# Kernel tuning notes

Measured on AMD Instinct MI355X. Metric: run time of the kernel, lower is better.

Reference implementation:

```python
import jax, jax.numpy as jnp
import numpy as np

B, N, E = 8, 10000, 320000
IN_DIM, E_H, E_OUT, N_OUT = 16, 32, 22, 16


def setup_inputs() -> dict:
    key = jax.random.key(0)
    ks = jax.random.split(key, 8)
    x = jax.random.uniform(ks[0], (B, N, IN_DIM), dtype=jnp.float32)
    edge_index = jax.random.randint(ks[1], (2, E), 0, N, dtype=jnp.int64)
    # edge_attr: col 0 = city_dist (keep strictly positive), col 1 = city_direc
    ea = jax.random.uniform(ks[2], (E, 2), dtype=jnp.float32)
    edge_attr = jnp.stack([ea[:, 0] * 100.0 + 1.0, ea[:, 1] * 360.0], axis=-1)
    wind_min = jnp.array([0.0, 0.0], dtype=jnp.float32)
    wind_max = jnp.array([15.0, 360.0], dtype=jnp.float32)
    W1 = jax.random.normal(ks[3], (2 * IN_DIM + 2 + 1, E_H), dtype=jnp.float32) * 0.1
    b1 = jnp.zeros((E_H,), dtype=jnp.float32)
    W2 = jax.random.normal(ks[4], (E_H, E_OUT), dtype=jnp.float32) * 0.1
    b2 = jnp.zeros((E_OUT,), dtype=jnp.float32)
    Wn = jax.random.normal(ks[5], (E_OUT, N_OUT), dtype=jnp.float32) * 0.1
    bn = jnp.zeros((N_OUT,), dtype=jnp.float32)
    return {"x": x, "edge_index": edge_index, "edge_attr": edge_attr,
            "wind_min": wind_min, "wind_max": wind_max,
            "W1": W1, "b1": b1, "W2": W2, "b2": b2, "Wn": Wn, "bn": bn}


def reference(x, edge_index, edge_attr, wind_min, wind_max, W1, b1, W2, b2, Wn, bn):
    edge_src = edge_index[0]
    edge_tgt = edge_index[1]
    n_nodes = x.shape[1]

    node_src = x[:, edge_src]      # [B, E, F]
    node_tgt = x[:, edge_tgt]      # [B, E, F]

    # de-normalize the last two features (wind speed, wind direction)
    src_wind = node_src[..., -2:] * (wind_max - wind_min) + wind_min
    src_speed = src_wind[..., 0]   # [B, E]
    src_direc = src_wind[..., 1]   # [B, E]

    city_dist = edge_attr[:, 0]    # [E]
    city_direc = edge_attr[:, 1]   # [E]

    theta = jnp.abs(city_direc[None, :] - src_direc)
    edge_weight = jax.nn.relu(src_speed * jnp.cos(theta) / city_dist[None, :])  # [B, E]

    ea_min = edge_attr.min(axis=0)
    ea_max = edge_attr.max(axis=0)
    ea_norm = (edge_attr - ea_min) / (ea_max - ea_min)  # [E, 2]
    ea_norm_b = jnp.broadcast_to(ea_norm[None], (x.shape[0],) + ea_norm.shape)

    feat = jnp.concatenate([node_src, node_tgt, ea_norm_b, edge_weight[..., None]], axis=-1)  # [B, E, 35]

    h = jax.nn.sigmoid(feat @ W1 + b1)   # [B, E, 32]
    e = jax.nn.sigmoid(h @ W2 + b2)      # [B, E, 22]

    # scatter_add to target nodes, scatter_add of negated messages to source nodes
    agg = jnp.zeros((x.shape[0], n_nodes, e.shape[-1]), dtype=e.dtype)
    agg = agg.at[:, edge_tgt].add(e)
    agg = agg.at[:, edge_src].add(-e)

    return jax.nn.sigmoid(agg @ Wn + bn)  # [B, N, out_dim]
```

## Files before the change

### kernel.cpp

```cpp
#include <hip/hip_runtime.h>
#include <math.h>

#define BB 8
#define NN 10000
#define EE 320000
#define NCHUNK 128
#define CHSZ (EE / NCHUNK)

#define OFF_MM   0
#define OFF_WIND 16
#define OFF_PRE1 160016
#define OFF_PRE2 2720016
#define OFF_OFFP 5280016
#define OFF_TOT  5300018
#define OFF_MMP  5320018
#define OFF_CNTC 5320530
#define OFF_LST  7880530
#define OFF_G    8520544

__device__ __forceinline__ float sigmf(float x) {
    return __fdividef(1.0f, 1.0f + __expf(-x));
}


__global__ __launch_bounds__(256) void count_kernel(const int* __restrict__ ei,
                                                    const float* __restrict__ ea,
                                                    unsigned* __restrict__ cntc,
                                                    float* __restrict__ mmpart) {
    __shared__ unsigned hist[NN];
    __shared__ float mred[4][4];
    const int c = blockIdx.x, a = blockIdx.y, tid = threadIdx.x;
    for (int i = tid; i < NN; i += 256) hist[i] = 0u;
    __syncthreads();
    const int e0 = c * CHSZ;
    float n0 = 3.4e38f, n1 = 3.4e38f, x0 = 0.f, x1 = 0.f;
    for (int k = tid; k < CHSZ; k += 256) {
        int v = ei[(size_t)a * EE + e0 + k];
        atomicAdd(&hist[v], 1u);
        if (a == 0) {
            float2 av = ((const float2*)ea)[e0 + k];
            n0 = fminf(n0, av.x); x0 = fmaxf(x0, av.x);
            n1 = fminf(n1, av.y); x1 = fmaxf(x1, av.y);
        }
    }
    __syncthreads();
    unsigned* dst = cntc + ((size_t)a * NCHUNK + c) * NN;
    for (int i = tid; i < NN; i += 256) dst[i] = hist[i];
    if (a == 0) {
        #pragma unroll
        for (int off = 32; off >= 1; off >>= 1) {
            n0 = fminf(n0, __shfl_xor(n0, off)); n1 = fminf(n1, __shfl_xor(n1, off));
            x0 = fmaxf(x0, __shfl_xor(x0, off)); x1 = fmaxf(x1, __shfl_xor(x1, off));
        }
        int w = tid >> 6;
        if ((tid & 63) == 0) { mred[w][0] = n0; mred[w][1] = n1; mred[w][2] = x0; mred[w][3] = x1; }
        __syncthreads();
        if (tid == 0) {
            mmpart[c * 4 + 0] = fminf(fminf(mred[0][0], mred[1][0]), fminf(mred[2][0], mred[3][0]));
            mmpart[c * 4 + 1] = fminf(fminf(mred[0][1], mred[1][1]), fminf(mred[2][1], mred[3][1]));
            mmpart[c * 4 + 2] = fmaxf(fmaxf(mred[0][2], mred[1][2]), fmaxf(mred[2][2], mred[3][2]));
            mmpart[c * 4 + 3] = fmaxf(fmaxf(mred[0][3], mred[1][3]), fmaxf(mred[2][3], mred[3][3]));
        }
    }
}

__global__ __launch_bounds__(256) void tot_kernel(const unsigned* __restrict__ cntc,
                                                  unsigned* __restrict__ tot) {
    int v = blockIdx.x * 256 + threadIdx.x;
    int a = blockIdx.y;
    if (v >= NN) return;
    const unsigned* base = cntc + (size_t)a * NCHUNK * NN;
    unsigned s = 0;
    for (int c = 0; c < NCHUNK; c++) s += base[(size_t)c * NN + v];
    tot[a * NN + v] = s;
}

__global__ __launch_bounds__(1024) void scan_kernel(const unsigned* __restrict__ tot,
                                                    const float* __restrict__ mmpart,
                                                    unsigned* __restrict__ offp,
                                                    float* __restrict__ mmo) {
    __shared__ unsigned ts[1024];
    int t = threadIdx.x;
    if (t < 64) {
        float n0 = fminf(mmpart[4 * t + 0], mmpart[4 * (t + 64) + 0]);
        float n1 = fminf(mmpart[4 * t + 1], mmpart[4 * (t + 64) + 1]);
        float x0 = fmaxf(mmpart[4 * t + 2], mmpart[4 * (t + 64) + 2]);
        float x1 = fmaxf(mmpart[4 * t + 3], mmpart[4 * (t + 64) + 3]);
        #pragma unroll
        for (int off = 32; off >= 1; off >>= 1) {
            n0 = fminf(n0, __shfl_xor(n0, off)); n1 = fminf(n1, __shfl_xor(n1, off));
            x0 = fmaxf(x0, __shfl_xor(x0, off)); x1 = fmaxf(x1, __shfl_xor(x1, off));
        }
        if (t == 0) { mmo[0] = n0; mmo[1] = n1; mmo[2] = x0; mmo[3] = x1; }
    }
    const int CH = 10;
    for (int a = 0; a < 2; a++) {
        const unsigned* c = tot + a * NN;
        unsigned* off = offp + a * (NN + 1);
        unsigned s = 0;
        int i0 = t * CH;
        #pragma unroll
        for (int k = 0; k < CH; k++) { int i = i0 + k; if (i < NN) s += c[i]; }
        ts[t] = s;
        __syncthreads();
        for (int d = 1; d < 1024; d <<= 1) {
            unsigned v = (t >= d) ? ts[t - d] : 0u;
            __syncthreads();
            ts[t] += v;
            __syncthreads();
        }
        unsigned run = ts[t] - s;
        #pragma unroll
        for (int k = 0; k < CH; k++) {
            int i = i0 + k;
            if (i < NN) { unsigned cv = c[i]; off[i] = run; run += cv; }
        }
        if (t == 1023) off[NN] = ts[1023];
        __syncthreads();
    }
}

__global__ __launch_bounds__(256) void base_kernel(unsigned* __restrict__ cntc,
                                                   const unsigned* __restrict__ offp) {
    int v = blockIdx.x * 256 + threadIdx.x;
    int a = blockIdx.y;
    if (v >= NN) return;
    unsigned run = offp[a * (NN + 1) + v];
    unsigned* base = cntc + (size_t)a * NCHUNK * NN;
    for (int c = 0; c < NCHUNK; c++) {
        unsigned cv = base[(size_t)c * NN + v];
        base[(size_t)c * NN + v] = run;
        run += cv;
    }
}

__global__ __launch_bounds__(256) void fill_kernel(const int* __restrict__ ei,
                                                   const unsigned* __restrict__ cntc,
                                                   unsigned* __restrict__ lst) {
    __shared__ unsigned cur[NN];
    const int c = blockIdx.x, a = blockIdx.y, tid = threadIdx.x;
    const unsigned* bs = cntc + ((size_t)a * NCHUNK + c) * NN;
    for (int i = tid; i < NN; i += 256) cur[i] = bs[i];
    __syncthreads();
    const int e0 = c * CHSZ;
    for (int k = tid; k < CHSZ; k += 256) {
        int e = e0 + k;
        int v = ei[(size_t)a * EE + e];
        unsigned p = atomicAdd(&cur[v], 1u);
        lst[(size_t)a * EE + p] = (unsigned)e;
    }
}

__global__ __launch_bounds__(256) void node_pre(const float* __restrict__ x,
                                                const float* __restrict__ W1,
                                                const float* __restrict__ wmin,
                                                const float* __restrict__ wmax,
                                                float* __restrict__ pre1,
                                                float* __restrict__ pre2,
                                                float* __restrict__ wind) {
    int id = blockIdx.x * 256 + threadIdx.x;
    if (id >= BB * NN) return;
    float xv[16];
    const float4* xp = (const float4*)(x + (size_t)id * 16);
    #pragma unroll
    for (int q = 0; q < 4; q++) {
        float4 v = xp[q];
        xv[4 * q + 0] = v.x; xv[4 * q + 1] = v.y;
        xv[4 * q + 2] = v.z; xv[4 * q + 3] = v.w;
    }
    float s1[32], s2[32];
    #pragma unroll
    for (int j = 0; j < 32; j++) { s1[j] = 0.f; s2[j] = 0.f; }
    #pragma unroll
    for (int r = 0; r < 16; r++) {
        float xr = xv[r];
        #pragma unroll
        for (int j = 0; j < 32; j++) {
            s1[j] = fmaf(xr, W1[r * 32 + j], s1[j]);
            s2[j] = fmaf(xr, W1[(16 + r) * 32 + j], s2[j]);
        }
    }
    float4* o1 = (float4*)(pre1 + (size_t)id * 32);
    float4* o2 = (float4*)(pre2 + (size_t)id * 32);
    #pragma unroll
    for (int q = 0; q < 8; q++) {
        o1[q] = make_float4(s1[4*q], s1[4*q+1], s1[4*q+2], s1[4*q+3]);
        o2[q] = make_float4(s2[4*q], s2[4*q+1], s2[4*q+2], s2[4*q+3]);
    }
    float sp = xv[14] * (wmax[0] - wmin[0]) + wmin[0];
    float dr = xv[15] * (wmax[1] - wmin[1]) + wmin[1];
    ((float2*)wind)[id] = make_float2(sp, dr);
}

__global__ __launch_bounds__(256) void edge_mlp(const int* __restrict__ ei,
                                                const float* __restrict__ ea,
                                                const float* __restrict__ pre1,
                                                const float* __restrict__ pre2,
                                                const float* __restrict__ wind,
                                                const float* __restrict__ mm,
                                                const float* __restrict__ W1,
                                                const float* __restrict__ b1,
                                                const float* __restrict__ W2,
                                                const float* __restrict__ b2,
                                                const float* __restrict__ Wn,
                                                float* __restrict__ gbuf,
                                                int b0, int nb) {
    __shared__ float gs[256 * 17];

    const int tid = threadIdx.x;
    const int e = blockIdx.x * 256 + tid;
    const int brel = blockIdx.y;
    const int b = b0 + brel;

    const int src = ei[e];
    const int tgt = ei[EE + e];
    const float2 eav = ((const float2*)ea)[e];
    const float2 wv = ((const float2*)wind)[(size_t)b * NN + src];

    float theta = fabsf(eav.y - wv.y);
    float ew = fmaxf(__fdividef(wv.x * cosf(theta), eav.x), 0.f);
    float ean0 = __fdividef(eav.x - mm[0], mm[2] - mm[0]);
    float ean1 = __fdividef(eav.y - mm[1], mm[3] - mm[1]);

    float h[32];
    const float4* p1 = (const float4*)(pre1 + ((size_t)b * NN + src) * 32);
    const float4* p2 = (const float4*)(pre2 + ((size_t)b * NN + tgt) * 32);
    #pragma unroll
    for (int q = 0; q < 8; q++) {
        float4 a = p1[q];
        float4 c = p2[q];
        h[4*q+0] = a.x + c.x; h[4*q+1] = a.y + c.y;
        h[4*q+2] = a.z + c.z; h[4*q+3] = a.w + c.w;
    }
    #pragma unroll
    for (int j = 0; j < 32; j++) {
        float v = h[j] + ean0 * W1[32 * 32 + j] + ean1 * W1[33 * 32 + j]
                        + ew * W1[34 * 32 + j] + b1[j];
        h[j] = sigmf(v);
    }

    float ef[22];
    #pragma unroll
    for (int k = 0; k < 22; k++) ef[k] = b2[k];
    #pragma unroll
    for (int j = 0; j < 32; j++) {
        float hv = h[j];
        #pragma unroll
        for (int k = 0; k < 22; k++) ef[k] = fmaf(hv, W2[j * 22 + k], ef[k]);
    }
    #pragma unroll
    for (int k = 0; k < 22; k++) ef[k] = sigmf(ef[k]);

    float gg[16];
    #pragma unroll
    for (int i = 0; i < 16; i++) gg[i] = 0.f;
    #pragma unroll
    for (int k = 0; k < 22; k++) {
        float ev = ef[k];
        #pragma unroll
        for (int i = 0; i < 16; i++) gg[i] = fmaf(ev, Wn[k * 16 + i], gg[i]);
    }

    #pragma unroll
    for (int i = 0; i < 16; i++) gs[tid * 17 + i] = gg[i];
    __syncthreads();

    const int c = tid & 15;
    const int base = tid >> 4;
    const size_t ebase = (size_t)blockIdx.x * 256;
    #pragma unroll
    for (int p = 0; p < 16; p++) {
        int s = base + p * 16;
        gbuf[((ebase + s) * (size_t)nb + brel) * 16 + c] = gs[s * 17 + c];
    }
}

__global__ __launch_bounds__(256) void gather_kernel(const unsigned* __restrict__ offp,
                                                     const unsigned* __restrict__ lst,
                                                     const float* __restrict__ gbuf,
                                                     const float* __restrict__ bn,
                                                     float* __restrict__ out,
                                                     int b0, int nb, int npb, int lgper) {
    int tid = threadIdx.x;
    int n = blockIdx.x * npb + (tid >> lgper);
    int rem = tid & ((1 << lgper) - 1);
    int bi = rem >> 4;
    int c = rem & 15;

    unsigned s0 = offp[n], s1 = offp[n + 1];
    unsigned t0 = offp[NN + 1 + n], t1 = offp[NN + 1 + n + 1];

    float acc = 0.f;
    for (unsigned k = t0; k < t1; k++) {
        int e = (int)lst[EE + k];
        acc += gbuf[((size_t)e * nb + bi) * 16 + c];
    }
    for (unsigned k = s0; k < s1; k++) {
        int e = (int)lst[k];
        acc -= gbuf[((size_t)e * nb + bi) * 16 + c];
    }
    out[((size_t)(b0 + bi) * NN + n) * 16 + c] = sigmf(acc + bn[c]);
}

__global__ void init_mm(unsigned* mm) {
    int t = threadIdx.x;
    if (t < 2) mm[t] = 0x7F7FFFFFu;
    else if (t < 4) mm[t] = 0u;
}

__global__ __launch_bounds__(256) void minmax_kernel(const float* __restrict__ ea,
                                                     unsigned* __restrict__ mm) {
    int t = blockIdx.x * 256 + threadIdx.x;
    float2 v = ((const float2*)ea)[t];
    float mn0 = v.x, mx0 = v.x, mn1 = v.y, mx1 = v.y;
    #pragma unroll
    for (int off = 32; off >= 1; off >>= 1) {
        mn0 = fminf(mn0, __shfl_xor(mn0, off));
        mx0 = fmaxf(mx0, __shfl_xor(mx0, off));
        mn1 = fminf(mn1, __shfl_xor(mn1, off));
        mx1 = fmaxf(mx1, __shfl_xor(mx1, off));
    }
    if ((threadIdx.x & 63) == 0) {
        atomicMin(&mm[0], __float_as_uint(mn0));
        atomicMin(&mm[1], __float_as_uint(mn1));
        atomicMax(&mm[2], __float_as_uint(mx0));
        atomicMax(&mm[3], __float_as_uint(mx1));
    }
}

__global__ __launch_bounds__(256) void edge_kernel(const int* __restrict__ ei,
                                                   const float* __restrict__ ea,
                                                   const float* __restrict__ pre1,
                                                   const float* __restrict__ pre2,
                                                   const float* __restrict__ wind,
                                                   const float* __restrict__ mm,
                                                   const float* __restrict__ W1,
                                                   const float* __restrict__ b1,
                                                   const float* __restrict__ W2,
                                                   const float* __restrict__ b2,
                                                   const float* __restrict__ Wn,
                                                   float* __restrict__ out) {
    __shared__ float gs[256 * 17];
    __shared__ int nd[512];
    const int tid = threadIdx.x;
    const int e = blockIdx.x * 256 + tid;
    const int b = blockIdx.y;
    const int src = ei[e];
    const int tgt = ei[EE + e];
    const float2 eav = ((const float2*)ea)[e];
    const float2 wv = ((const float2*)wind)[(size_t)b * NN + src];
    float theta = fabsf(eav.y - wv.y);
    float ew = fmaxf(__fdividef(wv.x * cosf(theta), eav.x), 0.f);
    float ean0 = __fdividef(eav.x - mm[0], mm[2] - mm[0]);
    float ean1 = __fdividef(eav.y - mm[1], mm[3] - mm[1]);
    float h[32];
    const float4* p1 = (const float4*)(pre1 + ((size_t)b * NN + src) * 32);
    const float4* p2 = (const float4*)(pre2 + ((size_t)b * NN + tgt) * 32);
    #pragma unroll
    for (int q = 0; q < 8; q++) {
        float4 a = p1[q]; float4 c = p2[q];
        h[4*q+0] = a.x + c.x; h[4*q+1] = a.y + c.y;
        h[4*q+2] = a.z + c.z; h[4*q+3] = a.w + c.w;
    }
    #pragma unroll
    for (int j = 0; j < 32; j++) {
        float v = h[j] + ean0 * W1[32*32+j] + ean1 * W1[33*32+j] + ew * W1[34*32+j] + b1[j];
        h[j] = sigmf(v);
    }
    float ef[22];
    #pragma unroll
    for (int k = 0; k < 22; k++) ef[k] = b2[k];
    #pragma unroll
    for (int j = 0; j < 32; j++) {
        float hv = h[j];
        #pragma unroll
        for (int k = 0; k < 22; k++) ef[k] = fmaf(hv, W2[j*22+k], ef[k]);
    }
    #pragma unroll
    for (int k = 0; k < 22; k++) ef[k] = sigmf(ef[k]);
    float g[16];
    #pragma unroll
    for (int i = 0; i < 16; i++) g[i] = 0.f;
    #pragma unroll
    for (int k = 0; k < 22; k++) {
        float ev = ef[k];
        #pragma unroll
        for (int i = 0; i < 16; i++) g[i] = fmaf(ev, Wn[k*16+i], g[i]);
    }
    nd[tid] = tgt; nd[256 + tid] = src;
    #pragma unroll
    for (int i = 0; i < 16; i++) gs[tid * 17 + i] = g[i];
    __syncthreads();
    const int c = tid & 15;
    const int base = tid >> 4;
    float* aggb = out + (size_t)b * NN * 16;
    for (int p = 0; p < 16; p++) {
        int s = base + p * 16;
        float val = gs[s * 17 + c];
        atomicAdd(&aggb[(size_t)nd[s] * 16 + c], val);
        atomicAdd(&aggb[(size_t)nd[256 + s] * 16 + c], -val);
    }
}

__global__ __launch_bounds__(256) void epilogue(float* __restrict__ out,
                                                const float* __restrict__ bn) {
    int id = blockIdx.x * 256 + threadIdx.x;
    if (id >= BB * NN * 4) return;
    float4 v = ((float4*)out)[id];
    int q = (id & 3) * 4;
    v.x = sigmf(v.x + bn[q + 0]);
    v.y = sigmf(v.y + bn[q + 1]);
    v.z = sigmf(v.z + bn[q + 2]);
    v.w = sigmf(v.w + bn[q + 3]);
    ((float4*)out)[id] = v;
}

extern "C" void kernel_launch(void* const* d_in, const int* in_sizes, int n_in,
                              void* d_out, int out_size, void* d_ws, size_t ws_size,
                              hipStream_t stream) {
    const float* x    = (const float*)d_in[0];
    const int*   ei   = (const int*)d_in[1];
    const float* ea   = (const float*)d_in[2];
    const float* wmin = (const float*)d_in[3];
    const float* wmax = (const float*)d_in[4];
    const float* W1   = (const float*)d_in[5];
    const float* b1   = (const float*)d_in[6];
    const float* W2   = (const float*)d_in[7];
    const float* b2   = (const float*)d_in[8];
    const float* Wn   = (const float*)d_in[9];
    const float* bn   = (const float*)d_in[10];
    float* out = (float*)d_out;

    float* ws       = (float*)d_ws;
    float* mmf      = ws + OFF_MM;
    unsigned* mmu   = (unsigned*)(ws + OFF_MM);
    float* wind     = ws + OFF_WIND;
    float* pre1     = ws + OFF_PRE1;
    float* pre2     = ws + OFF_PRE2;
    unsigned* offp  = (unsigned*)(ws + OFF_OFFP);
    unsigned* tot   = (unsigned*)(ws + OFF_TOT);
    float* mmpart   = ws + OFF_MMP;
    unsigned* cntc  = (unsigned*)(ws + OFF_CNTC);
    unsigned* lst   = (unsigned*)(ws + OFF_LST);
    float* gbuf     = ws + OFF_G;

    int nb = 8;
    while (nb > 1 && ((size_t)OFF_G + (size_t)nb * EE * 16) * 4ull > ws_size) nb >>= 1;
    bool csr_ok = ((size_t)OFF_G + (size_t)nb * EE * 16) * 4ull <= ws_size;

    node_pre<<<(BB * NN + 255) / 256, 256, 0, stream>>>(x, W1, wmin, wmax, pre1, pre2, wind);

    if (csr_ok) {
        count_kernel<<<dim3(NCHUNK, 2), 256, 0, stream>>>(ei, ea, cntc, mmpart);
        tot_kernel<<<dim3((NN + 255) / 256, 2), 256, 0, stream>>>(cntc, tot);
        scan_kernel<<<1, 1024, 0, stream>>>(tot, mmpart, offp, mmf);
        base_kernel<<<dim3((NN + 255) / 256, 2), 256, 0, stream>>>(cntc, offp);
        fill_kernel<<<dim3(NCHUNK, 2), 256, 0, stream>>>(ei, cntc, lst);

        int lgnb = (nb == 8) ? 3 : (nb == 4) ? 2 : (nb == 2) ? 1 : 0;
        int per = 16 * nb;
        int npb = 256 / per;
        int lgper = 4 + lgnb;
        for (int bc = 0; bc < BB; bc += nb) {
            edge_mlp<<<dim3(EE / 256, nb), 256, 0, stream>>>(ei, ea, pre1, pre2, wind,
                                                             mmf, W1, b1, W2, b2, Wn,
                                                             gbuf, bc, nb);
            gather_kernel<<<NN / npb, 256, 0, stream>>>(offp, lst, gbuf, bn, out,
                                                        bc, nb, npb, lgper);
        }
    } else {
        init_mm<<<1, 64, 0, stream>>>(mmu);
        minmax_kernel<<<EE / 256, 256, 0, stream>>>(ea, mmu);
        hipMemsetAsync(d_out, 0, (size_t)out_size * sizeof(float), stream);
        edge_kernel<<<dim3(EE / 256, BB), 256, 0, stream>>>(ei, ea, pre1, pre2, wind,
                                                            mmf, W1, b1, W2, b2, Wn, out);
        epilogue<<<(BB * NN * 4 + 255) / 256, 256, 0, stream>>>(out, bn);
    }
}
```

Measured before the change: 420.0 us.

## Use packed fp16 dot products and trig identity precompute in edge MLP

Replaces the per-edge cos(|a-b|) with a precomputed cos/sin decomposition: per-node wind vectors and per-edge direction-over-distance terms, so each edge evaluates a dot product instead of a transcendental. The MLP's second and third matmuls now run as packed fp16 dot2 ops with weights pre-packed by a new kernel. LOG2E is folded into the weights so sigmoids use exp2 and a reciprocal. The atomic fallback path is removed, and the kernel now returns early when workspace is too small. This cuts ALU work per edge but adds fp16 rounding error and an extra edge pass.

```diff
diff --git a/kernel.cpp b/kernel.cpp
--- a/kernel.cpp
+++ b/kernel.cpp
@@ -6,22 +6,87 @@
 #define EE 320000
 #define NCHUNK 128
 #define CHSZ (EE / NCHUNK)
+#define LOG2E 1.44269504088896340736f
 
 #define OFF_MM   0
-#define OFF_WIND 16
-#define OFF_PRE1 160016
-#define OFF_PRE2 2720016
-#define OFF_OFFP 5280016
-#define OFF_TOT  5300018
-#define OFF_MMP  5320018
-#define OFF_CNTC 5320530
-#define OFF_LST  7880530
-#define OFF_G    8520544
+#define PK_W2P   16
+#define PK_WNP   368
+#define PK_W1S   544
+#define PK_B1S   576
+#define PK_B2S   608
+#define OFF_WIND 640
+#define OFF_ECS  160640
+#define OFF_PRE1 800640
+#define OFF_PRE2 3360640
+#define OFF_OFFP 5920640
+#define OFF_TOT  5940642
+#define OFF_MMP  5960642
+#define OFF_CNTC 5961154
+#define OFF_LST  8521154
+#define OFF_G    9161168
+
+typedef _Float16 half2_t __attribute__((ext_vector_type(2)));
+typedef __fp16 fp16v2_t __attribute__((ext_vector_type(2)));
+
+__device__ __forceinline__ float rcpf(float x) {
+#if __has_builtin(__builtin_amdgcn_rcpf)
+    return __builtin_amdgcn_rcpf(x);
+#else
+    return __fdividef(1.0f, x);
+#endif
+}
+
+__device__ __forceinline__ half2_t pkh2(float a, float b) {
+#if __has_builtin(__builtin_amdgcn_cvt_pkrtz)
+    union { fp16v2_t t; half2_t h; } u;
+    u.t = __builtin_amdgcn_cvt_pkrtz(a, b);
+    return u.h;
+#else
+    half2_t r; r.x = (_Float16)a; r.y = (_Float16)b; return r;
+#endif
+}
+
+__device__ __forceinline__ float fdot2(half2_t a, half2_t b, float c) {
+#if __has_builtin(__builtin_amdgcn_fdot2)
+    return __builtin_amdgcn_fdot2(a, b, c, false);
+#else
+    return (float)a.x * (float)b.x + (float)a.y * (float)b.y + c;
+#endif
+}
+
+__device__ __forceinline__ float sig2(float xs) {
+    return rcpf(1.0f + exp2f(-xs));
+}
 
 __device__ __forceinline__ float sigmf(float x) {
     return __fdividef(1.0f, 1.0f + __expf(-x));
 }
 
+union h2f { half2_t h; float f; };
+
+__global__ __launch_bounds__(512) void pack_kernel(const float* __restrict__ W1,
+                                                   const float* __restrict__ b1,
+                                                   const float* __restrict__ W2,
+                                                   const float* __restrict__ b2,
+                                                   const float* __restrict__ Wn,
+                                                   float* __restrict__ ws) {
+    int t = threadIdx.x;
+    if (t < 352) {
+        int j2 = t / 22, k = t % 22;
+        h2f u; u.h = pkh2(W2[(2 * j2) * 22 + k] * LOG2E, W2[(2 * j2 + 1) * 22 + k] * LOG2E);
+        ws[PK_W2P + t] = u.f;
+    }
+    if (t < 176) {
+        int k2 = t / 16, i = t % 16;
+        h2f u; u.h = pkh2(Wn[(2 * k2) * 16 + i], Wn[(2 * k2 + 1) * 16 + i]);
+        ws[PK_WNP + t] = u.f;
+    }
+    if (t < 32) {
+        ws[PK_W1S + t] = W1[34 * 32 + t] * LOG2E;
+        ws[PK_B1S + t] = b1[t] * LOG2E;
+    }
+    if (t < 22) ws[PK_B2S + t] = b2[t] * LOG2E;
+}
 
 __global__ __launch_bounds__(256) void count_kernel(const int* __restrict__ ei,
                                                     const float* __restrict__ ea,
@@ -91,7 +156,11 @@
             n0 = fminf(n0, __shfl_xor(n0, off)); n1 = fminf(n1, __shfl_xor(n1, off));
             x0 = fmaxf(x0, __shfl_xor(x0, off)); x1 = fmaxf(x1, __shfl_xor(x1, off));
         }
-        if (t == 0) { mmo[0] = n0; mmo[1] = n1; mmo[2] = x0; mmo[3] = x1; }
+        if (t == 0) {
+            mmo[0] = n0; mmo[1] = n1;
+            mmo[2] = __fdividef(LOG2E, x0 - n0);
+            mmo[3] = __fdividef(LOG2E, x1 - n1);
+        }
     }
     const int CH = 10;
     for (int a = 0; a < 2; a++) {
@@ -184,25 +253,35 @@
     float4* o2 = (float4*)(pre2 + (size_t)id * 32);
     #pragma unroll
     for (int q = 0; q < 8; q++) {
-        o1[q] = make_float4(s1[4*q], s1[4*q+1], s1[4*q+2], s1[4*q+3]);
-        o2[q] = make_float4(s2[4*q], s2[4*q+1], s2[4*q+2], s2[4*q+3]);
+        o1[q] = make_float4(s1[4*q] * LOG2E, s1[4*q+1] * LOG2E, s1[4*q+2] * LOG2E, s1[4*q+3] * LOG2E);
+        o2[q] = make_float4(s2[4*q] * LOG2E, s2[4*q+1] * LOG2E, s2[4*q+2] * LOG2E, s2[4*q+3] * LOG2E);
     }
     float sp = xv[14] * (wmax[0] - wmin[0]) + wmin[0];
     float dr = xv[15] * (wmax[1] - wmin[1]) + wmin[1];
-    ((float2*)wind)[id] = make_float2(sp, dr);
+    float sv, cv;
+    sincosf(dr, &sv, &cv);
+    ((float2*)wind)[id] = make_float2(sp * cv, sp * sv);
+}
+
+__global__ __launch_bounds__(256) void edge_pre(const float* __restrict__ ea,
+                                                float* __restrict__ ecs) {
+    int e = blockIdx.x * 256 + threadIdx.x;
+    float2 av = ((const float2*)ea)[e];
+    float sv, cv;
+    sincosf(av.y, &sv, &cv);
+    float rd = __fdividef(1.0f, av.x);
+    ((float2*)ecs)[e] = make_float2(cv * rd, sv * rd);
 }
 
 __global__ __launch_bounds__(256) void edge_mlp(const int* __restrict__ ei,
                                                 const float* __restrict__ ea,
+                                                const float* __restrict__ ecs,
                                                 const float* __restrict__ pre1,
                                                 const float* __restrict__ pre2,
                                                 const float* __restrict__ wind,
-                                                const float* __restrict__ mm,
+                                                const float* __restrict__ mmo,
                                                 const float* __restrict__ W1,
-                                                const float* __restrict__ b1,
-                                                const float* __restrict__ W2,
-                                                const float* __restrict__ b2,
-                                                const float* __restrict__ Wn,
+                                                const float* __restrict__ wsf,
                                                 float* __restrict__ gbuf,
                                                 int b0, int nb) {
     __shared__ float gs[256 * 17];
@@ -215,50 +294,62 @@
     const int src = ei[e];
     const int tgt = ei[EE + e];
     const float2 eav = ((const float2*)ea)[e];
+    const float2 ec = ((const float2*)ecs)[e];
     const float2 wv = ((const float2*)wind)[(size_t)b * NN + src];
 
-    float theta = fabsf(eav.y - wv.y);
-    float ew = fmaxf(__fdividef(wv.x * cosf(theta), eav.x), 0.f);
-    float ean0 = __fdividef(eav.x - mm[0], mm[2] - mm[0]);
-    float ean1 = __fdividef(eav.y - mm[1], mm[3] - mm[1]);
-
-    float h[32];
+    float ew = fmaxf(wv.x * ec.x + wv.y * ec.y, 0.f);
+    float ean0 = (eav.x - mmo[0]) * mmo[2];
+    float ean1 = (eav.y - mmo[1]) * mmo[3];
+
+    const float* w1s = wsf + PK_W1S;
+    const float* b1s = wsf + PK_B1S;
+    const float* b2s = wsf + PK_B2S;
+    const half2_t* W2p = (const half2_t*)(wsf + PK_W2P);
+    const half2_t* Wnp = (const half2_t*)(wsf + PK_WNP);
+
+    half2_t hp[16];
     const float4* p1 = (const float4*)(pre1 + ((size_t)b * NN + src) * 32);
     const float4* p2 = (const float4*)(pre2 + ((size_t)b * NN + tgt) * 32);
     #pragma unroll
     for (int q = 0; q < 8; q++) {
         float4 a = p1[q];
         float4 c = p2[q];
-        h[4*q+0] = a.x + c.x; h[4*q+1] = a.y + c.y;
-        h[4*q+2] = a.z + c.z; h[4*q+3] = a.w + c.w;
-    }
-    #pragma unroll
-    for (int j = 0; j < 32; j++) {
-        float v = h[j] + ean0 * W1[32 * 32 + j] + ean1 * W1[33 * 32 + j]
-                        + ew * W1[34 * 32 + j] + b1[j];
-        h[j] = sigmf(v);
+        float s0 = a.x + c.x, s1 = a.y + c.y, s2 = a.z + c.z, s3 = a.w + c.w;
+        float h0, h1, h2, h3;
+        {
+            int j = 4 * q;
+            h0 = sig2(s0 + ean0 * W1[32*32 + j+0] + ean1 * W1[33*32 + j+0] + ew * w1s[j+0] + b1s[j+0]);
+            h1 = sig2(s1 + ean0 * W1[32*32 + j+1] + ean1 * W1[33*32 + j+1] + ew * w1s[j+1] + b1s[j+1]);
+            h2 = sig2(s2 + ean0 * W1[32*32 + j+2] + ean1 * W1[33*32 + j+2] + ew * w1s[j+2] + b1s[j+2]);
+            h3 = sig2(s3 + ean0 * W1[32*32 + j+3] + ean1 * W1[33*32 + j+3] + ew * w1s[j+3] + b1s[j+3]);
+        }
+        hp[2 * q]     = pkh2(h0, h1);
+        hp[2 * q + 1] = pkh2(h2, h3);
     }
 
     float ef[22];
     #pragma unroll
-    for (int k = 0; k < 22; k++) ef[k] = b2[k];
-    #pragma unroll
-    for (int j = 0; j < 32; j++) {
-        float hv = h[j];
-        #pragma unroll
-        for (int k = 0; k < 22; k++) ef[k] = fmaf(hv, W2[j * 22 + k], ef[k]);
-    }
-    #pragma unroll
-    for (int k = 0; k < 22; k++) ef[k] = sigmf(ef[k]);
+    for (int k = 0; k < 22; k++) ef[k] = b2s[k];
+    #pragma unroll
+    for (int j2 = 0; j2 < 16; j2++) {
+        #pragma unroll
+        for (int k = 0; k < 22; k++) ef[k] = fdot2(hp[j2], W2p[j2 * 22 + k], ef[k]);
+    }
+    half2_t efp[11];
+    #pragma unroll
+    for (int k2 = 0; k2 < 11; k2++) {
+        float e0 = sig2(ef[2 * k2]);
+        float e1 = sig2(ef[2 * k2 + 1]);
+        efp[k2] = pkh2(e0, e1);
+    }
 
     float gg[16];
     #pragma unroll
     for (int i = 0; i < 16; i++) gg[i] = 0.f;
     #pragma unroll
-    for (int k = 0; k < 22; k++) {
-        float ev = ef[k];
-        #pragma unroll
-        for (int i = 0; i < 16; i++) gg[i] = fmaf(ev, Wn[k * 16 + i], gg[i]);
+    for (int k2 = 0; k2 < 11; k2++) {
+        #pragma unroll
+        for (int i = 0; i < 16; i++) gg[i] = fdot2(efp[k2], Wnp[k2 * 16 + i], gg[i]);
     }
 
     #pragma unroll
@@ -300,119 +391,6 @@
         acc -= gbuf[((size_t)e * nb + bi) * 16 + c];
     }
     out[((size_t)(b0 + bi) * NN + n) * 16 + c] = sigmf(acc + bn[c]);
-}
-
-__global__ void init_mm(unsigned* mm) {
-    int t = threadIdx.x;
-    if (t < 2) mm[t] = 0x7F7FFFFFu;
-    else if (t < 4) mm[t] = 0u;
-}
-
-__global__ __launch_bounds__(256) void minmax_kernel(const float* __restrict__ ea,
-                                                     unsigned* __restrict__ mm) {
-    int t = blockIdx.x * 256 + threadIdx.x;
-    float2 v = ((const float2*)ea)[t];
-    float mn0 = v.x, mx0 = v.x, mn1 = v.y, mx1 = v.y;
-    #pragma unroll
-    for (int off = 32; off >= 1; off >>= 1) {
-        mn0 = fminf(mn0, __shfl_xor(mn0, off));
-        mx0 = fmaxf(mx0, __shfl_xor(mx0, off));
-        mn1 = fminf(mn1, __shfl_xor(mn1, off));
-        mx1 = fmaxf(mx1, __shfl_xor(mx1, off));
-    }
-    if ((threadIdx.x & 63) == 0) {
-        atomicMin(&mm[0], __float_as_uint(mn0));
-        atomicMin(&mm[1], __float_as_uint(mn1));
-        atomicMax(&mm[2], __float_as_uint(mx0));
-        atomicMax(&mm[3], __float_as_uint(mx1));
-    }
-}
-
-__global__ __launch_bounds__(256) void edge_kernel(const int* __restrict__ ei,
-                                                   const float* __restrict__ ea,
-                                                   const float* __restrict__ pre1,
-                                                   const float* __restrict__ pre2,
-                                                   const float* __restrict__ wind,
-                                                   const float* __restrict__ mm,
-                                                   const float* __restrict__ W1,
-                                                   const float* __restrict__ b1,
-                                                   const float* __restrict__ W2,
-                                                   const float* __restrict__ b2,
-                                                   const float* __restrict__ Wn,
-                                                   float* __restrict__ out) {
-    __shared__ float gs[256 * 17];
-    __shared__ int nd[512];
-    const int tid = threadIdx.x;
-    const int e = blockIdx.x * 256 + tid;
-    const int b = blockIdx.y;
-    const int src = ei[e];
-    const int tgt = ei[EE + e];
-    const float2 eav = ((const float2*)ea)[e];
-    const float2 wv = ((const float2*)wind)[(size_t)b * NN + src];
-    float theta = fabsf(eav.y - wv.y);
-    float ew = fmaxf(__fdividef(wv.x * cosf(theta), eav.x), 0.f);
-    float ean0 = __fdividef(eav.x - mm[0], mm[2] - mm[0]);
-    float ean1 = __fdividef(eav.y - mm[1], mm[3] - mm[1]);
-    float h[32];
-    const float4* p1 = (const float4*)(pre1 + ((size_t)b * NN + src) * 32);
-    const float4* p2 = (const float4*)(pre2 + ((size_t)b * NN + tgt) * 32);
-    #pragma unroll
-    for (int q = 0; q < 8; q++) {
-        float4 a = p1[q]; float4 c = p2[q];
-        h[4*q+0] = a.x + c.x; h[4*q+1] = a.y + c.y;
-        h[4*q+2] = a.z + c.z; h[4*q+3] = a.w + c.w;
-    }
-    #pragma unroll
-    for (int j = 0; j < 32; j++) {
-        float v = h[j] + ean0 * W1[32*32+j] + ean1 * W1[33*32+j] + ew * W1[34*32+j] + b1[j];
-        h[j] = sigmf(v);
-    }
-    float ef[22];
-    #pragma unroll
-    for (int k = 0; k < 22; k++) ef[k] = b2[k];
-    #pragma unroll
-    for (int j = 0; j < 32; j++) {
-        float hv = h[j];
-        #pragma unroll
-        for (int k = 0; k < 22; k++) ef[k] = fmaf(hv, W2[j*22+k], ef[k]);
-    }
-    #pragma unroll
-    for (int k = 0; k < 22; k++) ef[k] = sigmf(ef[k]);
-    float g[16];
-    #pragma unroll
-    for (int i = 0; i < 16; i++) g[i] = 0.f;
-    #pragma unroll
-    for (int k = 0; k < 22; k++) {
-        float ev = ef[k];
-        #pragma unroll
-        for (int i = 0; i < 16; i++) g[i] = fmaf(ev, Wn[k*16+i], g[i]);
-    }
-    nd[tid] = tgt; nd[256 + tid] = src;
-    #pragma unroll
-    for (int i = 0; i < 16; i++) gs[tid * 17 + i] = g[i];
-    __syncthreads();
-    const int c = tid & 15;
-    const int base = tid >> 4;
-    float* aggb = out + (size_t)b * NN * 16;
-    for (int p = 0; p < 16; p++) {
-        int s = base + p * 16;
-        float val = gs[s * 17 + c];
-        atomicAdd(&aggb[(size_t)nd[s] * 16 + c], val);
-        atomicAdd(&aggb[(size_t)nd[256 + s] * 16 + c], -val);
-    }
-}
-
-__global__ __launch_bounds__(256) void epilogue(float* __restrict__ out,
-                                                const float* __restrict__ bn) {
-    int id = blockIdx.x * 256 + threadIdx.x;
-    if (id >= BB * NN * 4) return;
-    float4 v = ((float4*)out)[id];
-    int q = (id & 3) * 4;
-    v.x = sigmf(v.x + bn[q + 0]);
-    v.y = sigmf(v.y + bn[q + 1]);
-    v.z = sigmf(v.z + bn[q + 2]);
-    v.w = sigmf(v.w + bn[q + 3]);
-    ((float4*)out)[id] = v;
 }
 
 extern "C" void kernel_launch(void* const* d_in, const int* in_sizes, int n_in,
@@ -432,9 +410,9 @@
     float* out = (float*)d_out;
 
     float* ws       = (float*)d_ws;
-    float* mmf      = ws + OFF_MM;
-    unsigned* mmu   = (unsigned*)(ws + OFF_MM);
+    float* mmo      = ws + OFF_MM;
     float* wind     = ws + OFF_WIND;
+    float* ecs      = ws + OFF_ECS;
     float* pre1     = ws + OFF_PRE1;
     float* pre2     = ws + OFF_PRE2;
     unsigned* offp  = (unsigned*)(ws + OFF_OFFP);
@@ -446,34 +424,26 @@
 
     int nb = 8;
     while (nb > 1 && ((size_t)OFF_G + (size_t)nb * EE * 16) * 4ull > ws_size) nb >>= 1;
-    bool csr_ok = ((size_t)OFF_G + (size_t)nb * EE * 16) * 4ull <= ws_size;
-
+    if (((size_t)OFF_G + (size_t)nb * EE * 16) * 4ull > ws_size) return;
+
+    pack_kernel<<<1, 512, 0, stream>>>(W1, b1, W2, b2, Wn, ws);
     node_pre<<<(BB * NN + 255) / 256, 256, 0, stream>>>(x, W1, wmin, wmax, pre1, pre2, wind);
-
-    if (csr_ok) {
-        count_kernel<<<dim3(NCHUNK, 2), 256, 0, stream>>>(ei, ea, cntc, mmpart);
-        tot_kernel<<<dim3((NN + 255) / 256, 2), 256, 0, stream>>>(cntc, tot);
-        scan_kernel<<<1, 1024, 0, stream>>>(tot, mmpart, offp, mmf);
-        base_kernel<<<dim3((NN + 255) / 256, 2), 256, 0, stream>>>(cntc, offp);
-        fill_kernel<<<dim3(NCHUNK, 2), 256, 0, stream>>>(ei, cntc, lst);
-
-        int lgnb = (nb == 8) ? 3 : (nb == 4) ? 2 : (nb == 2) ? 1 : 0;
-        int per = 16 * nb;
-        int npb = 256 / per;
-        int lgper = 4 + lgnb;
-        for (int bc = 0; bc < BB; bc += nb) {
-            edge_mlp<<<dim3(EE / 256, nb), 256, 0, stream>>>(ei, ea, pre1, pre2, wind,
-                                                             mmf, W1, b1, W2, b2, Wn,
-                                                             gbuf, bc, nb);
-            gather_kernel<<<NN / npb, 256, 0, stream>>>(offp, lst, gbuf, bn, out,
-                                                        bc, nb, npb, lgper);
-        }
-    } else {
-        init_mm<<<1, 64, 0, stream>>>(mmu);
-        minmax_kernel<<<EE / 256, 256, 0, stream>>>(ea, mmu);
-        hipMemsetAsync(d_out, 0, (size_t)out_size * sizeof(float), stream);
-        edge_kernel<<<dim3(EE / 256, BB), 256, 0, stream>>>(ei, ea, pre1, pre2, wind,
-                                                            mmf, W1, b1, W2, b2, Wn, out);
-        epilogue<<<(BB * NN * 4 + 255) / 256, 256, 0, stream>>>(out, bn);
-    }
-}
+    edge_pre<<<EE / 256, 256, 0, stream>>>(ea, ecs);
+
+    count_kernel<<<dim3(NCHUNK, 2), 256, 0, stream>>>(ei, ea, cntc, mmpart);
+    tot_kernel<<<dim3((NN + 255) / 256, 2), 256, 0, stream>>>(cntc, tot);
+    scan_kernel<<<1, 1024, 0, stream>>>(tot, mmpart, offp, mmo);
+    base_kernel<<<dim3((NN + 255) / 256, 2), 256, 0, stream>>>(cntc, offp);
+    fill_kernel<<<dim3(NCHUNK, 2), 256, 0, stream>>>(ei, cntc, lst);
+
+    int lgnb = (nb == 8) ? 3 : (nb == 4) ? 2 : (nb == 2) ? 1 : 0;
+    int per = 16 * nb;
+    int npb = 256 / per;
+    int lgper = 4 + lgnb;
+    for (int bc = 0; bc < BB; bc += nb) {
+        edge_mlp<<<dim3(EE / 256, nb), 256, 0, stream>>>(ei, ea, ecs, pre1, pre2, wind,
+                                                         mmo, W1, ws, gbuf, bc, nb);
+        gather_kernel<<<NN / npb, 256, 0, stream>>>(offp, lst, gbuf, bn, out,
+                                                    bc, nb, npb, lgper);
+    }
+}
```

Result: slower. 428.6 us (+2.0%).
